# Performance work log

Hardware: AMD Instinct MI355X
Metric: run time of the kernel (lower is better)

## Reference

```python
import jax, jax.numpy as jnp
import numpy as np

B, T, D, L, K = 16, 512, 256, 2, 3
MAX_OUT = 4096  # static padded output length = T * max_duration
LN_EPS = 1e-5


def setup_inputs() -> dict:
    key = jax.random.key(0)
    ks = jax.random.split(key, 8)
    x = jax.random.normal(ks[0], (B, T, D), dtype=jnp.float32)
    mfAlign = jax.random.randint(ks[1], (B, T), 0, 8, dtype=jnp.int32)  # integer frame durations
    pitch = jax.random.uniform(ks[2], (B, T), dtype=jnp.float32)
    energy = jax.random.uniform(ks[3], (B, T), dtype=jnp.float32)
    # duration Predictor params (2 conv layers + layernorms + final linear->1)
    conv_w = jax.random.normal(ks[4], (L, D, D, K), dtype=jnp.float32) * 0.02  # [layer, out, in, k]
    conv_b = jnp.zeros((L, D), dtype=jnp.float32)
    ln_g = jnp.ones((L, D), dtype=jnp.float32)
    ln_b = jnp.zeros((L, D), dtype=jnp.float32)
    lin_w = jax.random.normal(ks[5], (1, D), dtype=jnp.float32) * 0.02
    lin_b = jnp.zeros((1,), dtype=jnp.float32)
    return dict(x=x, mfAlign=mfAlign, pitch=pitch, energy=energy,
                conv_w=conv_w, conv_b=conv_b, ln_g=ln_g, ln_b=ln_b,
                lin_w=lin_w, lin_b=lin_b, max_out=MAX_OUT)


def _conv1d(h, w, b):
    # h: [B, T, D] -> NCW conv with same padding -> [B, T, D]
    y = jax.lax.conv_general_dilated(h.transpose(0, 2, 1), w, (1,), [(K // 2, K // 2)],
                                     dimension_numbers=('NCW', 'OIW', 'NCW'))
    return (y + b[None, :, None]).transpose(0, 2, 1)


def _layernorm(h, g, b):
    m = jnp.mean(h, axis=-1, keepdims=True)
    v = jnp.var(h, axis=-1, keepdims=True)
    return (h - m) * jax.lax.rsqrt(v + LN_EPS) * g + b


def _duration_predictor(h, conv_w, conv_b, ln_g, ln_b, lin_w, lin_b):
    # eval-mode Predictor: conv -> relu -> layernorm (dropout is identity at eval)
    for i in range(conv_w.shape[0]):
        h = _layernorm(jax.nn.relu(_conv1d(h, conv_w[i], conv_b[i])), ln_g[i], ln_b[i])
    return (h @ lin_w.T + lin_b)[..., 0]  # [B, T]


def _length_regulator(x, dur, max_out):
    # expand token t of batch b dur[b,t] times; pad each row to max_out
    dur = jnp.maximum(dur, 0)
    cum = jnp.cumsum(dur, axis=1)                 # [B, T]
    lengths = cum[:, -1]                          # [B]
    pos = jnp.arange(max_out, dtype=cum.dtype)    # [max_out]
    # output frame p of batch b copies token idx[b,p] = first t with cum[b,t] > p
    idx = jax.vmap(lambda c: jnp.searchsorted(c, pos, side='right'))(cum)
    idx = jnp.minimum(idx, x.shape[1] - 1)
    hidden = jnp.take_along_axis(x, idx[:, :, None], axis=1)   # [B, max_out, D]
    mask = (pos[None, :] < lengths[:, None])[:, :, None]
    return jnp.where(mask, hidden, jnp.zeros((), x.dtype)), lengths


def reference(x, mfAlign, pitch, energy, conv_w, conv_b, ln_g, ln_b, lin_w, lin_b, max_out):
    # VarianceAdaptor.forward with bGenerating=False
    lab = mfAlign.astype(x.dtype)
    d = _duration_predictor(jax.lax.stop_gradient(x), conv_w, conv_b, ln_g, ln_b, lin_w, lin_b)
    dLoss = jnp.mean((d - lab) ** 2)
    hiddenSeq, hiddenSeqLength = _length_regulator(x, mfAlign, max_out)
    return hiddenSeq, hiddenSeqLength, dLoss
```

## Files before the change

kernel.cpp:

```cpp
#include <hip/hip_runtime.h>
#include <hip/hip_bf16.h>

#define DD 256
#define TTT 512
#define BB 16
#define KK 3
#define MAXO 4096
#define LN_EPS 1e-5f
#define TPAD 514
#define NKT 24

typedef __attribute__((ext_vector_type(8))) short short8;
typedef __attribute__((ext_vector_type(4))) float f32x4;

static __device__ inline short bf16r(float v) {
    __hip_bfloat16 h = __float2bfloat16(v);
    return reinterpret_cast<short&>(h);
}

__global__ __launch_bounds__(512) void k_prep_all(
    const float* __restrict__ x, const int* __restrict__ mf,
    const float* __restrict__ w, short* __restrict__ wpk,
    short* __restrict__ xb, short* __restrict__ h1b,
    int* __restrict__ cum, int* __restrict__ idxb, float* __restrict__ dout) {
    __shared__ int s[TTT];
    int blk = blockIdx.x;
    if (blk < 16) {
        int b = blk, t = threadIdx.x;
        s[t] = mf[b * TTT + t];
        __syncthreads();
        for (int off = 1; off < TTT; off <<= 1) {
            int v = (t >= off) ? s[t - off] : 0;
            __syncthreads();
            s[t] += v;
            __syncthreads();
        }
        cum[b * TTT + t] = s[t];
        int hi = s[t];
        int lo = (t == 0) ? 0 : s[t - 1];
        for (int p = lo; p < hi; ++p) idxb[b * MAXO + p] = t;
        if (t == TTT - 1) dout[(size_t)BB * MAXO * DD + b] = (float)s[t];
        if (b == 0 && t == 0) dout[(size_t)BB * MAXO * DD + BB] = 0.f;
    } else if (blk < 112) {
        int tid = (blk - 16) * 512 + threadIdx.x;
        int lane = tid & 63;
        int rest = tid >> 6;
        int nf = rest & 15; rest >>= 4;
        int kt = rest % NKT;
        int l  = rest / NKT;
        int n     = nf * 16 + (lane & 15);
        int kbase = kt * 32 + (lane >> 4) * 8;
        short8 v;
#pragma unroll
        for (int j = 0; j < 8; ++j) {
            int k   = kbase + j;
            int kap = k >> 8;
            int i   = k & 255;
            v[j] = bf16r(w[(((l * DD) + n) * DD + i) * KK + kap]);
        }
        *reinterpret_cast<short8*>(wpk + (size_t)tid * 8) = v;
    } else {
        int tid = (blk - 112) * 512 + threadIdx.x;
        int r = (tid >> 8) % TPAD;
        if (r == 0 || r == TPAD - 1) {
            xb[tid] = 0; h1b[tid] = 0;
        } else {
            int c = tid & 255;
            int b = tid / (TPAD * DD);
            xb[tid] = bf16r(x[((size_t)b * TTT + (r - 1)) * DD + c]);
        }
    }
}

template <bool DO_LOSS>
static __device__ inline void conv_body(
    int bt, int tid,
    const short* __restrict__ ain, short* __restrict__ aout,
    const short8* __restrict__ bp, const float* __restrict__ cb,
    const float* __restrict__ g, const float* __restrict__ bvec,
    const float* __restrict__ lw, const float* __restrict__ lb,
    const int* __restrict__ mf, float* __restrict__ loss,
    float (*yt)[260]) {
    int b  = bt >> 5;
    int t0 = (bt & 31) << 4;
    int lane = tid & 63, wv = tid >> 6;
    int mrow = lane & 15;
    int kg   = lane >> 4;

    const short* Ab = ain + ((size_t)b * TPAD + t0 + mrow) * DD + kg * 8;
    f32x4 acc0 = {0.f,0.f,0.f,0.f}, acc1 = acc0, acc2 = acc0, acc3 = acc0;
    const short8* bw = bp + (size_t)wv * 4 * 64 + lane;

    for (int kt = 0; kt < NKT; ++kt) {
        short8 a  = *reinterpret_cast<const short8*>(Ab + kt * 32);
        short8 b0 = bw[0];
        short8 b1 = bw[64];
        short8 b2 = bw[128];
        short8 b3 = bw[192];
        acc0 = __builtin_amdgcn_mfma_f32_16x16x32_bf16(a, b0, acc0, 0, 0, 0);
        acc1 = __builtin_amdgcn_mfma_f32_16x16x32_bf16(a, b1, acc1, 0, 0, 0);
        acc2 = __builtin_amdgcn_mfma_f32_16x16x32_bf16(a, b2, acc2, 0, 0, 0);
        acc3 = __builtin_amdgcn_mfma_f32_16x16x32_bf16(a, b3, acc3, 0, 0, 0);
        bw += 16 * 64;
    }

#define EPI(F, ACC) { int c = ((wv * 4 + F) << 4) + mrow; float bias = cb[c];   \
        yt[kg * 4 + 0][c] = fmaxf(ACC[0] + bias, 0.f);                          \
        yt[kg * 4 + 1][c] = fmaxf(ACC[1] + bias, 0.f);                          \
        yt[kg * 4 + 2][c] = fmaxf(ACC[2] + bias, 0.f);                          \
        yt[kg * 4 + 3][c] = fmaxf(ACC[3] + bias, 0.f); }
    EPI(0, acc0) EPI(1, acc1) EPI(2, acc2) EPI(3, acc3)
#undef EPI
    __syncthreads();

    float lsum = 0.f;
    int c0 = lane << 1;
#pragma unroll
    for (int q = 0; q < 4; ++q) {
        int r = wv * 4 + q;
        float2 vA = *reinterpret_cast<float2*>(&yt[r][c0]);
        float2 vB = *reinterpret_cast<float2*>(&yt[r][c0 + 128]);
        float s  = vA.x + vA.y + vB.x + vB.y;
        float s2 = vA.x*vA.x + vA.y*vA.y + vB.x*vB.x + vB.y*vB.y;
#pragma unroll
        for (int off = 1; off < 64; off <<= 1) {
            s  += __shfl_xor(s, off);
            s2 += __shfl_xor(s2, off);
        }
        float mean = s * (1.f / DD);
        float var  = s2 * (1.f / DD) - mean * mean;
        float rs   = rsqrtf(var + LN_EPS);
        float2 gA = *reinterpret_cast<const float2*>(&g[c0]);
        float2 gB = *reinterpret_cast<const float2*>(&g[c0 + 128]);
        float2 bA = *reinterpret_cast<const float2*>(&bvec[c0]);
        float2 bB = *reinterpret_cast<const float2*>(&bvec[c0 + 128]);
        float oAx = (vA.x - mean) * rs * gA.x + bA.x;
        float oAy = (vA.y - mean) * rs * gA.y + bA.y;
        float oBx = (vB.x - mean) * rs * gB.x + bB.x;
        float oBy = (vB.y - mean) * rs * gB.y + bB.y;
        if constexpr (!DO_LOSS) {
            size_t rowb = ((size_t)b * TPAD + t0 + r + 1) * DD;
            short2 sA, sB;
            sA.x = bf16r(oAx); sA.y = bf16r(oAy);
            sB.x = bf16r(oBx); sB.y = bf16r(oBy);
            *reinterpret_cast<short2*>(&aout[rowb + c0])       = sA;
            *reinterpret_cast<short2*>(&aout[rowb + c0 + 128]) = sB;
        } else {
            float2 lA = *reinterpret_cast<const float2*>(&lw[c0]);
            float2 lB = *reinterpret_cast<const float2*>(&lw[c0 + 128]);
            float p = oAx * lA.x + oAy * lA.y + oBx * lB.x + oBy * lB.y;
#pragma unroll
            for (int off = 1; off < 64; off <<= 1) p += __shfl_xor(p, off);
            if (lane == 0) {
                float dv = p + lb[0];
                float er = dv - (float)mf[b * TTT + t0 + r];
                lsum += er * er;
            }
        }
    }
    if constexpr (DO_LOSS) {
        if (lane == 0) atomicAdd(loss, lsum * (1.f / (BB * TTT)));
    }
}

__global__ __launch_bounds__(256) void k_mid(
    const short* __restrict__ xb, short* __restrict__ h1b,
    const short8* __restrict__ bp, const float* __restrict__ cb,
    const float* __restrict__ g, const float* __restrict__ bvec,
    const float* __restrict__ x, const int* __restrict__ cum,
    const int* __restrict__ idxb, float* __restrict__ out) {
    __shared__ float yt[16][260];
    int blk = blockIdx.x;
    int tid = threadIdx.x;
    if (blk < 512) {
        conv_body<false>(blk, tid, xb, h1b, bp, cb, g, bvec,
                         nullptr, nullptr, nullptr, nullptr, yt);
    } else {
        int lrb = blk - 512;
        int b   = lrb >> 7;
        int p0  = (lrb & 127) << 5;
        int lane = tid & 63, wv = tid >> 6;
        int len = cum[b * TTT + TTT - 1];
        const float4* x4 = (const float4*)x;
        float4* o4 = (float4*)out;
#pragma unroll
        for (int r = 0; r < 8; ++r) {
            int p = p0 + (wv << 3) + r;
            size_t oidx = ((size_t)b * MAXO + p) * 64 + lane;
            if (p < len) {
                int idx = idxb[b * MAXO + p];
                o4[oidx] = x4[((size_t)b * TTT + idx) * 64 + lane];
            } else {
                o4[oidx] = make_float4(0.f, 0.f, 0.f, 0.f);
            }
        }
    }
}

__global__ __launch_bounds__(256) void k_final(
    const short* __restrict__ h1b, const short8* __restrict__ bp,
    const float* __restrict__ cb, const float* __restrict__ g,
    const float* __restrict__ bvec, const float* __restrict__ lw,
    const float* __restrict__ lb, const int* __restrict__ mf,
    float* __restrict__ loss) {
    __shared__ float yt[16][260];
    conv_body<true>(blockIdx.x, threadIdx.x, h1b, nullptr, bp, cb, g, bvec,
                    lw, lb, mf, loss, yt);
}

extern "C" void kernel_launch(void* const* d_in, const int* in_sizes, int n_in,
                              void* d_out, int out_size, void* d_ws, size_t ws_size,
                              hipStream_t stream) {
    const float* x      = (const float*)d_in[0];
    const int*   mf     = (const int*)d_in[1];
    const float* conv_w = (const float*)d_in[4];
    const float* conv_b = (const float*)d_in[5];
    const float* ln_g   = (const float*)d_in[6];
    const float* ln_b   = (const float*)d_in[7];
    const float* lin_w  = (const float*)d_in[8];
    const float* lin_b  = (const float*)d_in[9];
    float* out = (float*)d_out;

    short* wpk = (short*)d_ws;
    short* xb  = wpk + (size_t)2 * NKT * 16 * 64 * 8;
    short* h1b = xb + (size_t)BB * TPAD * DD;
    int*   cum  = (int*)(h1b + (size_t)BB * TPAD * DD);
    int*   idxb = cum + BB * TTT;

    float* lossp = out + (size_t)BB * MAXO * DD + BB;

    k_prep_all<<<16 + 96 + 4112, 512, 0, stream>>>(
        x, mf, conv_w, wpk, xb, h1b, cum, idxb, out);
    k_mid<<<512 + BB * (MAXO / 32), 256, 0, stream>>>(
        xb, h1b, (const short8*)wpk, conv_b, ln_g, ln_b,
        x, cum, idxb, out);
    k_final<<<512, 256, 0, stream>>>(
        h1b, (const short8*)wpk + (size_t)NKT * 16 * 64,
        conv_b + DD, ln_g + DD, ln_b + DD, lin_w, lin_b, mf, lossp);
}
```

Baseline: 158.6 us.

## Vectorize bf16 padding conversion and schedule length-regulator blocks before conv blocks

The x-to-bf16 padded conversion in the prep kernel now has each thread handle 8 elements, using two float4 loads and one short8 store, so the grid shrinks from 4112 to 514 conversion blocks. In the mid kernel the block order is swapped: the 2048 memory-bound length-regulator copy blocks take the low block indices and the 512 conv blocks come after them. The goal is fewer, wider memory transactions, plus a different overlap between the bandwidth-heavy gather and the compute-heavy conv work. Conv blocks now launch last, which could lengthen the critical path if they become the tail.

```diff
diff --git a/kernel.cpp b/kernel.cpp
--- a/kernel.cpp
+++ b/kernel.cpp
@@ -60,14 +60,24 @@
         }
         *reinterpret_cast<short8*>(wpk + (size_t)tid * 8) = v;
     } else {
-        int tid = (blk - 112) * 512 + threadIdx.x;
-        int r = (tid >> 8) % TPAD;
+        int t8 = (blk - 112) * 512 + threadIdx.x;
+        int rowg = t8 >> 5;
+        int c0   = (t8 & 31) << 3;
+        int r = rowg % TPAD;
+        int b = rowg / TPAD;
+        size_t o8 = (size_t)t8 * 8;
         if (r == 0 || r == TPAD - 1) {
-            xb[tid] = 0; h1b[tid] = 0;
+            short8 z = {0,0,0,0,0,0,0,0};
+            *reinterpret_cast<short8*>(xb + o8)  = z;
+            *reinterpret_cast<short8*>(h1b + o8) = z;
         } else {
-            int c = tid & 255;
-            int b = tid / (TPAD * DD);
-            xb[tid] = bf16r(x[((size_t)b * TTT + (r - 1)) * DD + c]);
+            const float* src = x + ((size_t)b * TTT + (r - 1)) * DD + c0;
+            float4 fA = *reinterpret_cast<const float4*>(src);
+            float4 fB = *reinterpret_cast<const float4*>(src + 4);
+            short8 v;
+            v[0] = bf16r(fA.x); v[1] = bf16r(fA.y); v[2] = bf16r(fA.z); v[3] = bf16r(fA.w);
+            v[4] = bf16r(fB.x); v[5] = bf16r(fB.y); v[6] = bf16r(fB.z); v[7] = bf16r(fB.w);
+            *reinterpret_cast<short8*>(xb + o8) = v;
         }
     }
 }
@@ -172,13 +182,12 @@
     __shared__ float yt[16][260];
     int blk = blockIdx.x;
     int tid = threadIdx.x;
-    if (blk < 512) {
-        conv_body<false>(blk, tid, xb, h1b, bp, cb, g, bvec,
+    if (blk >= 2048) {
+        conv_body<false>(blk - 2048, tid, xb, h1b, bp, cb, g, bvec,
                          nullptr, nullptr, nullptr, nullptr, yt);
     } else {
-        int lrb = blk - 512;
-        int b   = lrb >> 7;
-        int p0  = (lrb & 127) << 5;
+        int b   = blk >> 7;
+        int p0  = (blk & 127) << 5;
         int lane = tid & 63, wv = tid >> 6;
         int len = cum[b * TTT + TTT - 1];
         const float4* x4 = (const float4*)x;
@@ -229,9 +238,9 @@
 
     float* lossp = out + (size_t)BB * MAXO * DD + BB;
 
-    k_prep_all<<<16 + 96 + 4112, 512, 0, stream>>>(
+    k_prep_all<<<16 + 96 + 514, 512, 0, stream>>>(
         x, mf, conv_w, wpk, xb, h1b, cum, idxb, out);
-    k_mid<<<512 + BB * (MAXO / 32), 256, 0, stream>>>(
+    k_mid<<<2048 + 512, 256, 0, stream>>>(
         xb, h1b, (const short8*)wpk, conv_b, ln_g, ln_b,
         x, cum, idxb, out);
     k_final<<<512, 256, 0, stream>>>(
```

New measurement: 170.1 us. 1.07x slower.
